# Kernel optimization log

Measured on AMD Instinct MI355X. Metric: run time of the kernel, lower is better.

## Reference

```python
import jax, jax.numpy as jnp
import numpy as np

N_NODES = 50000
N_EDGES = 800000
IN_F = 64
OUT_F = 64
HEADS = 4
ALPHA = 0.2  # LeakyReLU negative slope


def setup_inputs() -> dict:
    key = jax.random.key(0)
    k1, k2, k3, k4, k5, k6 = jax.random.split(key, 6)
    x = jax.random.normal(k1, (N_NODES, IN_F), dtype=jnp.float32)
    src = jax.random.randint(k2, (N_EDGES,), 0, N_NODES)
    dst = jax.random.randint(k3, (N_EDGES,), 0, N_NODES)
    edge_index = jnp.stack([src, dst]).astype(jnp.int64)
    # learned params: per-head projection + attention vectors (GAT)
    W = jax.random.normal(k4, (HEADS, IN_F, OUT_F), dtype=jnp.float32) * 0.1
    a_src = jax.random.normal(k5, (HEADS, OUT_F), dtype=jnp.float32) * 0.1
    a_dst = jax.random.normal(k6, (HEADS, OUT_F), dtype=jnp.float32) * 0.1
    return {"x": x, "edge_index": edge_index, "W": W, "a_src": a_src, "a_dst": a_dst}


def reference(x, edge_index, W, a_src, a_dst):
    N = x.shape[0]
    src, dst = edge_index[0], edge_index[1]
    # per-head projection: [N, H, O]
    h = jnp.einsum('nf,hfo->nho', x, W)
    # node-level attention halves: [N, H]
    s_src = jnp.einsum('nho,ho->nh', h, a_src)
    s_dst = jnp.einsum('nho,ho->nh', h, a_dst)
    # edge logits with LeakyReLU: [E, H]
    e = jax.nn.leaky_relu(s_src[src] + s_dst[dst], negative_slope=ALPHA)
    # segment softmax over incoming edges of each destination node
    e_max = jax.ops.segment_max(e, dst, num_segments=N)  # [N, H]
    e_exp = jnp.exp(e - e_max[dst])
    denom = jax.ops.segment_sum(e_exp, dst, num_segments=N)  # [N, H]
    attn = e_exp / (denom[dst] + 1e-16)  # [E, H]
    # weighted scatter-aggregation: [N, H, O]
    msg = h[src] * attn[:, :, None]
    out = jax.ops.segment_sum(msg, dst, num_segments=N)
    # average_head=False -> concatenate heads; no bias, no activation
    return out.reshape(N, HEADS * OUT_F)
```

## Files before the change

### kernel.cpp

```cpp
#include <hip/hip_runtime.h>

#define HEADS 4
#define OUTF 64
#define INF 64
#define CAP 48
#define DSTR 16

typedef __attribute__((ext_vector_type(8))) short bf16x8;
typedef __attribute__((ext_vector_type(4))) float f32x4;

__device__ __forceinline__ ushort f2bf(float f) {
    const unsigned u = __float_as_uint(f);
    return (ushort)((u + 0x7fffu + ((u >> 16) & 1u)) >> 16);
}

__global__ __launch_bounds__(256) void prep_kernel(
    const float* __restrict__ W, const float* __restrict__ a_src,
    const float* __restrict__ a_dst, float* __restrict__ va_s, float* __restrict__ va_d,
    ushort* __restrict__ W_packed, const int* __restrict__ ei, int* __restrict__ flag)
{
    const int t = threadIdx.x;
    if (blockIdx.x == 8) {
        if (t == 0) {
            int all0 = 1;
            #pragma unroll
            for (int k = 1; k < 64; k += 2) all0 &= (ei[k] == 0);
            *flag = all0;
        }
        const int h = t >> 6;
        const float* Wr = W + (size_t)t * 64;
        const float* as = a_src + h * 64;
        const float* ad = a_dst + h * 64;
        float s = 0.f, d = 0.f;
        #pragma unroll
        for (int o = 0; o < 64; ++o) {
            const float wv = Wr[o];
            s = fmaf(wv, as[o], s);
            d = fmaf(wv, ad[o], d);
        }
        va_s[t] = s;
        va_d[t] = d;
        return;
    }
    const int idx  = blockIdx.x * 256 + t;
    const int tile = idx >> 7;
    const int st   = (idx >> 6) & 1;
    const int l    = idx & 63;
    const int o_g  = tile * 16 + (l & 15);
    const int hh   = o_g >> 6;
    const int oo   = o_g & 63;
    const int k0   = st * 32 + (l >> 4) * 8;
    ushort v[8];
    #pragma unroll
    for (int i = 0; i < 8; ++i)
        v[i] = f2bf(W[(size_t)hh * 4096 + (size_t)(k0 + i) * 64 + oo]);
    uint4 u;
    u.x = v[0] | ((unsigned)v[1] << 16);
    u.y = v[2] | ((unsigned)v[3] << 16);
    u.z = v[4] | ((unsigned)v[5] << 16);
    u.w = v[6] | ((unsigned)v[7] << 16);
    *reinterpret_cast<uint4*>(W_packed + (size_t)idx * 8) = u;
}

__global__ __launch_bounds__(256) void s_fill_kernel(
    const float* __restrict__ x, const float* __restrict__ va_s,
    const float* __restrict__ va_d, float* __restrict__ ssrc,
    float* __restrict__ sdst, ushort* __restrict__ x_bf,
    const int* __restrict__ ei, const int* __restrict__ flag,
    int* __restrict__ deg, ushort* __restrict__ csr_src, int N, int E)
{
    const int nid = blockIdx.x * 256 + threadIdx.x;
    if (nid < N) {
        const float* xr = x + (size_t)nid * 64;
        float rs[4] = {0.f, 0.f, 0.f, 0.f};
        float rd[4] = {0.f, 0.f, 0.f, 0.f};
        #pragma unroll
        for (int f4 = 0; f4 < 16; ++f4) {
            const float4 xv = *reinterpret_cast<const float4*>(xr + 4 * f4);
            uint2 xb;
            xb.x = f2bf(xv.x) | ((unsigned)f2bf(xv.y) << 16);
            xb.y = f2bf(xv.z) | ((unsigned)f2bf(xv.w) << 16);
            *reinterpret_cast<uint2*>(x_bf + (size_t)nid * 64 + 4 * f4) = xb;
            #pragma unroll
            for (int h = 0; h < 4; ++h) {
                const float4 s4 = *reinterpret_cast<const float4*>(va_s + h * 64 + 4 * f4);
                const float4 d4 = *reinterpret_cast<const float4*>(va_d + h * 64 + 4 * f4);
                rs[h] = fmaf(xv.x, s4.x, fmaf(xv.y, s4.y, fmaf(xv.z, s4.z, fmaf(xv.w, s4.w, rs[h]))));
                rd[h] = fmaf(xv.x, d4.x, fmaf(xv.y, d4.y, fmaf(xv.z, d4.z, fmaf(xv.w, d4.w, rd[h]))));
            }
        }
        *reinterpret_cast<float4*>(ssrc + (size_t)nid * 4) = make_float4(rs[0], rs[1], rs[2], rs[3]);
        *reinterpret_cast<float4*>(sdst + (size_t)nid * 4) = make_float4(rd[0], rd[1], rd[2], rd[3]);
    }
    const int i64v = *flag;
    const int P4 = E >> 2;
    const int stride = gridDim.x * 256;
    for (int p = blockIdx.x * 256 + threadIdx.x; p < P4; p += stride) {
        int s0, s1, s2, s3, d0, d1, d2, d3;
        if (i64v) {
            const int4 sa = *reinterpret_cast<const int4*>(ei + 8 * (size_t)p);
            const int4 sb = *reinterpret_cast<const int4*>(ei + 8 * (size_t)p + 4);
            const int4 da = *reinterpret_cast<const int4*>(ei + 2 * (size_t)E + 8 * (size_t)p);
            const int4 db = *reinterpret_cast<const int4*>(ei + 2 * (size_t)E + 8 * (size_t)p + 4);
            s0 = sa.x; s1 = sa.z; s2 = sb.x; s3 = sb.z;
            d0 = da.x; d1 = da.z; d2 = db.x; d3 = db.z;
        } else {
            const int4 sv = *reinterpret_cast<const int4*>(ei + 4 * (size_t)p);
            const int4 dv = *reinterpret_cast<const int4*>(ei + (size_t)E + 4 * (size_t)p);
            s0 = sv.x; s1 = sv.y; s2 = sv.z; s3 = sv.w;
            d0 = dv.x; d1 = dv.y; d2 = dv.z; d3 = dv.w;
        }
        const int p0 = atomicAdd(&deg[(size_t)d0 * DSTR], 1);
        const int p1 = atomicAdd(&deg[(size_t)d1 * DSTR], 1);
        const int p2 = atomicAdd(&deg[(size_t)d2 * DSTR], 1);
        const int p3 = atomicAdd(&deg[(size_t)d3 * DSTR], 1);
        if (p0 < CAP) csr_src[(size_t)d0 * CAP + p0] = (ushort)s0;
        if (p1 < CAP) csr_src[(size_t)d1 * CAP + p1] = (ushort)s1;
        if (p2 < CAP) csr_src[(size_t)d2 * CAP + p2] = (ushort)s2;
        if (p3 < CAP) csr_src[(size_t)d3 * CAP + p3] = (ushort)s3;
    }
    if (blockIdx.x == 0 && threadIdx.x == 0) {
        for (int i = E & ~3; i < E; ++i) {
            int src, dst;
            if (i64v) { src = ei[2 * (size_t)i]; dst = ei[2 * ((size_t)E + i)]; }
            else      { src = ei[i];             dst = ei[(size_t)E + i]; }
            const int pos = atomicAdd(&deg[(size_t)dst * DSTR], 1);
            if (pos < CAP) csr_src[(size_t)dst * CAP + pos] = (ushort)src;
        }
    }
}

#define ACCUM(XV, SS) do { \
    float e0 = (SS).x + sd4.x, e1 = (SS).y + sd4.y, e2 = (SS).z + sd4.z, e3 = (SS).w + sd4.w; \
    e0 = e0 >= 0.f ? e0 : 0.2f * e0; \
    e1 = e1 >= 0.f ? e1 : 0.2f * e1; \
    e2 = e2 >= 0.f ? e2 : 0.2f * e2; \
    e3 = e3 >= 0.f ? e3 : 0.2f * e3; \
    const float w0 = __expf(e0), w1 = __expf(e1), w2 = __expf(e2), w3 = __expf(e3); \
    const float f0 = __uint_as_float((XV).x << 16); \
    const float f1 = __uint_as_float((XV).x & 0xffff0000u); \
    const float f2 = __uint_as_float((XV).y << 16); \
    const float f3 = __uint_as_float((XV).y & 0xffff0000u); \
    A00 = fmaf(w0, f0, A00); A01 = fmaf(w0, f1, A01); A02 = fmaf(w0, f2, A02); A03 = fmaf(w0, f3, A03); \
    A10 = fmaf(w1, f0, A10); A11 = fmaf(w1, f1, A11); A12 = fmaf(w1, f2, A12); A13 = fmaf(w1, f3, A13); \
    A20 = fmaf(w2, f0, A20); A21 = fmaf(w2, f1, A21); A22 = fmaf(w2, f2, A22); A23 = fmaf(w2, f3, A23); \
    A30 = fmaf(w3, f0, A30); A31 = fmaf(w3, f1, A31); A32 = fmaf(w3, f2, A32); A33 = fmaf(w3, f3, A33); \
    ws0 += w0; ws1 += w1; ws2 += w2; ws3 += w3; \
} while (0)

#define CHUNK(SV, CNT) do { \
    int j = 0; \
    for (; j + 2 <= (CNT); j += 2) { \
        const int sA = __shfl((SV), g0 + j); \
        const int sB = __shfl((SV), g0 + j + 1); \
        const uint2 xA = *reinterpret_cast<const uint2*>(x_bf + ((size_t)sA << 6) + (l4 << 2)); \
        const uint2 xB = *reinterpret_cast<const uint2*>(x_bf + ((size_t)sB << 6) + (l4 << 2)); \
        const float4 pA = *reinterpret_cast<const float4*>(ssrc + 4 * (size_t)sA); \
        const float4 pB = *reinterpret_cast<const float4*>(ssrc + 4 * (size_t)sB); \
        ACCUM(xA, pA); \
        ACCUM(xB, pB); \
    } \
    if (j < (CNT)) { \
        const int sA = __shfl((SV), g0 + j); \
        const uint2 xA = *reinterpret_cast<const uint2*>(x_bf + ((size_t)sA << 6) + (l4 << 2)); \
        const float4 pA = *reinterpret_cast<const float4*>(ssrc + 4 * (size_t)sA); \
        ACCUM(xA, pA); \
    } \
} while (0)

__global__ __launch_bounds__(256) void gather_agg(
    const int* __restrict__ deg, const ushort* __restrict__ csr_src,
    const ushort* __restrict__ x_bf, const float* __restrict__ ssrc,
    const float* __restrict__ sdst, ushort* __restrict__ agg_bf, int N)
{
    const int tid  = threadIdx.x;
    const int lane = tid & 63;
    const int l4   = lane & 15;
    const int g0   = lane & 48;
    const int n    = blockIdx.x * 16 + (tid >> 6) * 4 + (lane >> 4);
    const size_t base = (size_t)n * CAP;
    const int d    = min(deg[(size_t)n * DSTR], CAP);

    const int sv0 = (int)csr_src[base + l4];
    const int sv1 = (int)csr_src[base + 16 + l4];
    const int sv2 = (int)csr_src[base + 32 + l4];

    const float4 sd4 = *reinterpret_cast<const float4*>(sdst + (size_t)n * 4);

    float A00 = 0.f, A01 = 0.f, A02 = 0.f, A03 = 0.f;
    float A10 = 0.f, A11 = 0.f, A12 = 0.f, A13 = 0.f;
    float A20 = 0.f, A21 = 0.f, A22 = 0.f, A23 = 0.f;
    float A30 = 0.f, A31 = 0.f, A32 = 0.f, A33 = 0.f;
    float ws0 = 0.f, ws1 = 0.f, ws2 = 0.f, ws3 = 0.f;

    const int c0 = min(d, 16);
    const int c1 = min(max(d - 16, 0), 16);
    const int c2 = min(max(d - 32, 0), 16);
    CHUNK(sv0, c0);
    CHUNK(sv1, c1);
    CHUNK(sv2, c2);

    ushort* ap = agg_bf + ((size_t)n << 8) + (l4 << 2);
    const float i0 = 1.f / (ws0 + 1e-16f);
    const float i1 = 1.f / (ws1 + 1e-16f);
    const float i2 = 1.f / (ws2 + 1e-16f);
    const float i3 = 1.f / (ws3 + 1e-16f);
    uint2 o;
    o.x = f2bf(A00 * i0) | ((unsigned)f2bf(A01 * i0) << 16);
    o.y = f2bf(A02 * i0) | ((unsigned)f2bf(A03 * i0) << 16);
    *reinterpret_cast<uint2*>(ap) = o;
    o.x = f2bf(A10 * i1) | ((unsigned)f2bf(A11 * i1) << 16);
    o.y = f2bf(A12 * i1) | ((unsigned)f2bf(A13 * i1) << 16);
    *reinterpret_cast<uint2*>(ap + 64) = o;
    o.x = f2bf(A20 * i2) | ((unsigned)f2bf(A21 * i2) << 16);
    o.y = f2bf(A22 * i2) | ((unsigned)f2bf(A23 * i2) << 16);
    *reinterpret_cast<uint2*>(ap + 128) = o;
    o.x = f2bf(A30 * i3) | ((unsigned)f2bf(A31 * i3) << 16);
    o.y = f2bf(A32 * i3) | ((unsigned)f2bf(A33 * i3) << 16);
    *reinterpret_cast<uint2*>(ap + 192) = o;
}

__global__ __launch_bounds__(256) void out_mfma(
    const ushort* __restrict__ agg_bf, const ushort* __restrict__ W_packed,
    float* __restrict__ out, int nNodes)
{
    const int t    = threadIdx.x;
    const int wave = t >> 6;
    const int lane = t & 63;
    const int n0   = blockIdx.x * 32;
    const int r    = lane & 15;
    const int kb   = (lane >> 4) * 8;
    const int ar0  = min(n0 + r, nNodes - 1);
    const int ar1  = min(n0 + 16 + r, nNodes - 1);
    const size_t hoff = (size_t)wave * 64;

    const bf16x8 a00 = *reinterpret_cast<const bf16x8*>(agg_bf + ((size_t)ar0 << 8) + hoff + kb);
    const bf16x8 a01 = *reinterpret_cast<const bf16x8*>(agg_bf + ((size_t)ar0 << 8) + hoff + 32 + kb);
    const bf16x8 a10 = *reinterpret_cast<const bf16x8*>(agg_bf + ((size_t)ar1 << 8) + hoff + kb);
    const bf16x8 a11 = *reinterpret_cast<const bf16x8*>(agg_bf + ((size_t)ar1 << 8) + hoff + 32 + kb);

    const int drow = (lane >> 4) * 4;
    #pragma unroll
    for (int tt = 0; tt < 4; ++tt) {
        const int tile = wave * 4 + tt;
        const bf16x8 b0 = *reinterpret_cast<const bf16x8*>(W_packed + ((size_t)(tile * 2 + 0) * 64 + lane) * 8);
        const bf16x8 b1 = *reinterpret_cast<const bf16x8*>(W_packed + ((size_t)(tile * 2 + 1) * 64 + lane) * 8);
        f32x4 acc0 = {0.f, 0.f, 0.f, 0.f};
        f32x4 acc1 = {0.f, 0.f, 0.f, 0.f};
        acc0 = __builtin_amdgcn_mfma_f32_16x16x32_bf16(a00, b0, acc0, 0, 0, 0);
        acc0 = __builtin_amdgcn_mfma_f32_16x16x32_bf16(a01, b1, acc0, 0, 0, 0);
        acc1 = __builtin_amdgcn_mfma_f32_16x16x32_bf16(a10, b0, acc1, 0, 0, 0);
        acc1 = __builtin_amdgcn_mfma_f32_16x16x32_bf16(a11, b1, acc1, 0, 0, 0);
        const int col = tile * 16 + r;
        #pragma unroll
        for (int i = 0; i < 4; ++i) {
            const int na  = n0 + drow + i;
            const int nb2 = na + 16;
            if (na  < nNodes) out[(size_t)na  * 256 + col] = acc0[i];
            if (nb2 < nNodes) out[(size_t)nb2 * 256 + col] = acc1[i];
        }
    }
}

extern "C" void kernel_launch(void* const* d_in, const int* in_sizes, int n_in,
                              void* d_out, int out_size, void* d_ws, size_t ws_size,
                              hipStream_t stream) {
    const float* x     = (const float*)d_in[0];
    const int*   ei    = (const int*)d_in[1];
    const float* W     = (const float*)d_in[2];
    const float* a_src = (const float*)d_in[3];
    const float* a_dst = (const float*)d_in[4];
    float*       out   = (float*)d_out;

    const int N = in_sizes[0] / INF;
    const int E = in_sizes[1] / 2;

    ushort* agg_bf   = (ushort*)d_ws;
    ushort* x_bf     = agg_bf + (size_t)N * 256;
    ushort* W_packed = x_bf + (size_t)N * 64;
    float* ssrc      = (float*)(W_packed + 16384);
    float* sdst      = ssrc + (size_t)N * 4;
    float* va_s      = sdst + (size_t)N * 4;
    float* va_d      = va_s + 256;
    int*   deg       = (int*)(va_d + 256);
    ushort* csr_src  = (ushort*)(deg + (size_t)N * DSTR);
    int*   flag      = (int*)(csr_src + (size_t)N * CAP);

    const int nblk_fill = ((E >> 2) + 255) / 256;

    hipMemsetAsync(deg, 0, (size_t)N * DSTR * sizeof(int), stream);
    prep_kernel<<<9, 256, 0, stream>>>(W, a_src, a_dst, va_s, va_d, W_packed, ei, flag);
    s_fill_kernel<<<nblk_fill, 256, 0, stream>>>(x, va_s, va_d, ssrc, sdst, x_bf, ei, flag, deg, csr_src, N, E);
    gather_agg<<<N / 16, 256, 0, stream>>>(deg, csr_src, x_bf, ssrc, sdst, agg_bf, N);
    out_mfma<<<(N + 31) / 32, 256, 0, stream>>>(agg_bf, W_packed, out, N);
}
```

Measured before the change: 102.7 us.

## Fuse gather aggregation with output MFMA via LDS and widen edge fill

Merges the attention-weighted gather and the per-head output projection into one kernel. Each block stores its 16 normalized aggregate rows in shared memory and runs the MFMA directly from there, so the bf16 aggregate buffer is no longer written to and read back from global memory and one launch is dropped. The CSR fill loop now handles 8 edges per thread, issuing more independent atomics per thread. The trade-off is one MFMA row tile per block instead of two, extra LDS use, and half as many fill blocks.

```diff
diff --git a/kernel.cpp b/kernel.cpp
--- a/kernel.cpp
+++ b/kernel.cpp
@@ -93,34 +93,35 @@
         *reinterpret_cast<float4*>(sdst + (size_t)nid * 4) = make_float4(rd[0], rd[1], rd[2], rd[3]);
     }
     const int i64v = *flag;
-    const int P4 = E >> 2;
+    const int P8 = E >> 3;
     const int stride = gridDim.x * 256;
-    for (int p = blockIdx.x * 256 + threadIdx.x; p < P4; p += stride) {
-        int s0, s1, s2, s3, d0, d1, d2, d3;
+    for (int p = blockIdx.x * 256 + threadIdx.x; p < P8; p += stride) {
+        int s[8], d[8], pos[8];
         if (i64v) {
-            const int4 sa = *reinterpret_cast<const int4*>(ei + 8 * (size_t)p);
-            const int4 sb = *reinterpret_cast<const int4*>(ei + 8 * (size_t)p + 4);
-            const int4 da = *reinterpret_cast<const int4*>(ei + 2 * (size_t)E + 8 * (size_t)p);
-            const int4 db = *reinterpret_cast<const int4*>(ei + 2 * (size_t)E + 8 * (size_t)p + 4);
-            s0 = sa.x; s1 = sa.z; s2 = sb.x; s3 = sb.z;
-            d0 = da.x; d1 = da.z; d2 = db.x; d3 = db.z;
+            #pragma unroll
+            for (int q = 0; q < 4; ++q) {
+                const int4 sv = *reinterpret_cast<const int4*>(ei + 16 * (size_t)p + 4 * q);
+                const int4 dv = *reinterpret_cast<const int4*>(ei + 2 * (size_t)E + 16 * (size_t)p + 4 * q);
+                s[2 * q] = sv.x; s[2 * q + 1] = sv.z;
+                d[2 * q] = dv.x; d[2 * q + 1] = dv.z;
+            }
         } else {
-            const int4 sv = *reinterpret_cast<const int4*>(ei + 4 * (size_t)p);
-            const int4 dv = *reinterpret_cast<const int4*>(ei + (size_t)E + 4 * (size_t)p);
-            s0 = sv.x; s1 = sv.y; s2 = sv.z; s3 = sv.w;
-            d0 = dv.x; d1 = dv.y; d2 = dv.z; d3 = dv.w;
-        }
-        const int p0 = atomicAdd(&deg[(size_t)d0 * DSTR], 1);
-        const int p1 = atomicAdd(&deg[(size_t)d1 * DSTR], 1);
-        const int p2 = atomicAdd(&deg[(size_t)d2 * DSTR], 1);
-        const int p3 = atomicAdd(&deg[(size_t)d3 * DSTR], 1);
-        if (p0 < CAP) csr_src[(size_t)d0 * CAP + p0] = (ushort)s0;
-        if (p1 < CAP) csr_src[(size_t)d1 * CAP + p1] = (ushort)s1;
-        if (p2 < CAP) csr_src[(size_t)d2 * CAP + p2] = (ushort)s2;
-        if (p3 < CAP) csr_src[(size_t)d3 * CAP + p3] = (ushort)s3;
+            #pragma unroll
+            for (int q = 0; q < 2; ++q) {
+                const int4 sv = *reinterpret_cast<const int4*>(ei + 8 * (size_t)p + 4 * q);
+                const int4 dv = *reinterpret_cast<const int4*>(ei + (size_t)E + 8 * (size_t)p + 4 * q);
+                s[4 * q] = sv.x; s[4 * q + 1] = sv.y; s[4 * q + 2] = sv.z; s[4 * q + 3] = sv.w;
+                d[4 * q] = dv.x; d[4 * q + 1] = dv.y; d[4 * q + 2] = dv.z; d[4 * q + 3] = dv.w;
+            }
+        }
+        #pragma unroll
+        for (int k = 0; k < 8; ++k) pos[k] = atomicAdd(&deg[(size_t)d[k] * DSTR], 1);
+        #pragma unroll
+        for (int k = 0; k < 8; ++k)
+            if (pos[k] < CAP) csr_src[(size_t)d[k] * CAP + pos[k]] = (ushort)s[k];
     }
     if (blockIdx.x == 0 && threadIdx.x == 0) {
-        for (int i = E & ~3; i < E; ++i) {
+        for (int i = E & ~7; i < E; ++i) {
             int src, dst;
             if (i64v) { src = ei[2 * (size_t)i]; dst = ei[2 * ((size_t)E + i)]; }
             else      { src = ei[i];             dst = ei[(size_t)E + i]; }
@@ -168,16 +169,21 @@
     } \
 } while (0)
 
-__global__ __launch_bounds__(256) void gather_agg(
+__global__ __launch_bounds__(256) void gather_out(
     const int* __restrict__ deg, const ushort* __restrict__ csr_src,
     const ushort* __restrict__ x_bf, const float* __restrict__ ssrc,
-    const float* __restrict__ sdst, ushort* __restrict__ agg_bf, int N)
+    const float* __restrict__ sdst, const ushort* __restrict__ W_packed,
+    float* __restrict__ out, int N)
 {
+    __shared__ ushort agg_lds[16][264];
+
     const int tid  = threadIdx.x;
     const int lane = tid & 63;
     const int l4   = lane & 15;
     const int g0   = lane & 48;
-    const int n    = blockIdx.x * 16 + (tid >> 6) * 4 + (lane >> 4);
+    const int wv   = tid >> 6;
+    const int nl   = wv * 4 + (lane >> 4);
+    const int n    = blockIdx.x * 16 + nl;
     const size_t base = (size_t)n * CAP;
     const int d    = min(deg[(size_t)n * DSTR], CAP);
 
@@ -200,7 +206,7 @@
     CHUNK(sv1, c1);
     CHUNK(sv2, c2);
 
-    ushort* ap = agg_bf + ((size_t)n << 8) + (l4 << 2);
+    ushort* ap = &agg_lds[nl][l4 << 2];
     const float i0 = 1.f / (ws0 + 1e-16f);
     const float i1 = 1.f / (ws1 + 1e-16f);
     const float i2 = 1.f / (ws2 + 1e-16f);
@@ -218,47 +224,29 @@
     o.x = f2bf(A30 * i3) | ((unsigned)f2bf(A31 * i3) << 16);
     o.y = f2bf(A32 * i3) | ((unsigned)f2bf(A33 * i3) << 16);
     *reinterpret_cast<uint2*>(ap + 192) = o;
-}
-
-__global__ __launch_bounds__(256) void out_mfma(
-    const ushort* __restrict__ agg_bf, const ushort* __restrict__ W_packed,
-    float* __restrict__ out, int nNodes)
-{
-    const int t    = threadIdx.x;
-    const int wave = t >> 6;
-    const int lane = t & 63;
-    const int n0   = blockIdx.x * 32;
+
+    __syncthreads();
+
     const int r    = lane & 15;
     const int kb   = (lane >> 4) * 8;
-    const int ar0  = min(n0 + r, nNodes - 1);
-    const int ar1  = min(n0 + 16 + r, nNodes - 1);
-    const size_t hoff = (size_t)wave * 64;
-
-    const bf16x8 a00 = *reinterpret_cast<const bf16x8*>(agg_bf + ((size_t)ar0 << 8) + hoff + kb);
-    const bf16x8 a01 = *reinterpret_cast<const bf16x8*>(agg_bf + ((size_t)ar0 << 8) + hoff + 32 + kb);
-    const bf16x8 a10 = *reinterpret_cast<const bf16x8*>(agg_bf + ((size_t)ar1 << 8) + hoff + kb);
-    const bf16x8 a11 = *reinterpret_cast<const bf16x8*>(agg_bf + ((size_t)ar1 << 8) + hoff + 32 + kb);
+    const int hoff = wv * 64;
+    const bf16x8 a0 = *reinterpret_cast<const bf16x8*>(&agg_lds[r][hoff + kb]);
+    const bf16x8 a1 = *reinterpret_cast<const bf16x8*>(&agg_lds[r][hoff + 32 + kb]);
 
     const int drow = (lane >> 4) * 4;
+    const int nb0  = blockIdx.x * 16;
     #pragma unroll
     for (int tt = 0; tt < 4; ++tt) {
-        const int tile = wave * 4 + tt;
+        const int tile = wv * 4 + tt;
         const bf16x8 b0 = *reinterpret_cast<const bf16x8*>(W_packed + ((size_t)(tile * 2 + 0) * 64 + lane) * 8);
         const bf16x8 b1 = *reinterpret_cast<const bf16x8*>(W_packed + ((size_t)(tile * 2 + 1) * 64 + lane) * 8);
-        f32x4 acc0 = {0.f, 0.f, 0.f, 0.f};
-        f32x4 acc1 = {0.f, 0.f, 0.f, 0.f};
-        acc0 = __builtin_amdgcn_mfma_f32_16x16x32_bf16(a00, b0, acc0, 0, 0, 0);
-        acc0 = __builtin_amdgcn_mfma_f32_16x16x32_bf16(a01, b1, acc0, 0, 0, 0);
-        acc1 = __builtin_amdgcn_mfma_f32_16x16x32_bf16(a10, b0, acc1, 0, 0, 0);
-        acc1 = __builtin_amdgcn_mfma_f32_16x16x32_bf16(a11, b1, acc1, 0, 0, 0);
+        f32x4 acc = {0.f, 0.f, 0.f, 0.f};
+        acc = __builtin_amdgcn_mfma_f32_16x16x32_bf16(a0, b0, acc, 0, 0, 0);
+        acc = __builtin_amdgcn_mfma_f32_16x16x32_bf16(a1, b1, acc, 0, 0, 0);
         const int col = tile * 16 + r;
         #pragma unroll
-        for (int i = 0; i < 4; ++i) {
-            const int na  = n0 + drow + i;
-            const int nb2 = na + 16;
-            if (na  < nNodes) out[(size_t)na  * 256 + col] = acc0[i];
-            if (nb2 < nNodes) out[(size_t)nb2 * 256 + col] = acc1[i];
-        }
+        for (int i = 0; i < 4; ++i)
+            out[(size_t)(nb0 + drow + i) * 256 + col] = acc[i];
     }
 }
 
@@ -275,8 +263,7 @@
     const int N = in_sizes[0] / INF;
     const int E = in_sizes[1] / 2;
 
-    ushort* agg_bf   = (ushort*)d_ws;
-    ushort* x_bf     = agg_bf + (size_t)N * 256;
+    ushort* x_bf     = (ushort*)d_ws;
     ushort* W_packed = x_bf + (size_t)N * 64;
     float* ssrc      = (float*)(W_packed + 16384);
     float* sdst      = ssrc + (size_t)N * 4;
@@ -286,11 +273,10 @@
     ushort* csr_src  = (ushort*)(deg + (size_t)N * DSTR);
     int*   flag      = (int*)(csr_src + (size_t)N * CAP);
 
-    const int nblk_fill = ((E >> 2) + 255) / 256;
+    const int nblk_fill = ((E >> 3) + 255) / 256;
 
     hipMemsetAsync(deg, 0, (size_t)N * DSTR * sizeof(int), stream);
     prep_kernel<<<9, 256, 0, stream>>>(W, a_src, a_dst, va_s, va_d, W_packed, ei, flag);
     s_fill_kernel<<<nblk_fill, 256, 0, stream>>>(x, va_s, va_d, ssrc, sdst, x_bf, ei, flag, deg, csr_src, N, E);
-    gather_agg<<<N / 16, 256, 0, stream>>>(deg, csr_src, x_bf, ssrc, sdst, agg_bf, N);
-    out_mfma<<<(N + 31) / 32, 256, 0, stream>>>(agg_bf, W_packed, out, N);
-}
+    gather_out<<<N / 16, 256, 0, stream>>>(deg, csr_src, x_bf, ssrc, sdst, W_packed, out, N);
+}
```

New measurement: 91.73 us. -10.7%, faster.
